# Performance work log

Measured on AMD Instinct MI355X. Metric: run time of the kernel, lower is better.

The kernel has to match this reference:

```python
import jax, jax.numpy as jnp
import numpy as np
from jax import lax

T, H, F, E, K = 4096, 1024, 2048, 8, 2

def setup_inputs() -> dict:
    key = jax.random.key(0)
    k1, k2, k3, k4 = jax.random.split(key, 4)
    return {
        "hidden_states": jax.random.normal(k1, (T, H), jnp.float32),
        "gate_w": jax.random.normal(k2, (E, H), jnp.float32) * 0.02,
        "w1": jax.random.normal(k3, (E, 2 * F, H), jnp.float32) * 0.02,  # fused gate+up
        "w2": jax.random.normal(k4, (E, H, F), jnp.float32) * 0.02,      # down proj
        "top_k": K,
    }

def reference(hidden_states, gate_w, w1, w2, top_k):
    tokens = hidden_states.shape[0]
    # Router gate (Linear, no bias)
    router_logits = hidden_states @ gate_w.T                     # [T, E]
    probs = jax.nn.softmax(router_logits.astype(jnp.float32), axis=-1)
    topk_w, topk_idx = lax.top_k(probs, top_k)                   # [T, K]
    topk_w = topk_w / jnp.sum(topk_w, axis=-1, keepdims=True)    # renormalize
    # Dense combine weights [T, E] (zero for unselected experts)
    combine = jnp.zeros_like(probs).at[jnp.arange(tokens)[:, None], topk_idx].add(topk_w)
    combine = combine.astype(hidden_states.dtype)

    def expert_step(acc, ew):
        w1_e, w2_e, c_e = ew                                     # [2F,H], [H,F], [T]
        h = hidden_states @ w1_e.T                               # [T, 2F]
        g, u = jnp.split(h, 2, axis=-1)
        y = (jax.nn.silu(g) * u) @ w2_e.T                        # [T, H]
        return acc + c_e[:, None] * y, None

    acc0 = jnp.zeros_like(hidden_states)
    final_hidden_states, _ = lax.scan(expert_step, acc0, (w1, w2, combine.T))
    return final_hidden_states, router_logits
```

## Files before the change

kernel.cpp:

```cpp
#include <hip/hip_runtime.h>

#define T 4096
#define Hdim 1024
#define Fdim 2048
#define NE 8
#define TOPK 2
#define TK (T*TOPK)

typedef unsigned short ushort_t;
typedef __attribute__((ext_vector_type(8))) short bf16x8;
typedef __attribute__((ext_vector_type(4))) float floatx4;

__device__ __forceinline__ ushort_t f2bf(float f) {
    unsigned u = __float_as_uint(f);
    u += 0x7fff + ((u >> 16) & 1);
    return (ushort_t)(u >> 16);
}
__device__ __forceinline__ uint4 cvt8(const float4 a, const float4 b) {
    uint4 r;
    r.x = (unsigned)f2bf(a.x) | ((unsigned)f2bf(a.y) << 16);
    r.y = (unsigned)f2bf(a.z) | ((unsigned)f2bf(a.w) << 16);
    r.z = (unsigned)f2bf(b.x) | ((unsigned)f2bf(b.y) << 16);
    r.w = (unsigned)f2bf(b.z) | ((unsigned)f2bf(b.w) << 16);
    return r;
}
__device__ __forceinline__ void gld16(const ushort_t* g, short* l) {
    __builtin_amdgcn_global_load_lds((const __attribute__((address_space(1))) void*)g,
                                     (__attribute__((address_space(3))) void*)l, 16, 0, 0);
}

__global__ __launch_bounds__(256) void cvt_kernel(const float* __restrict__ src,
                                                  ushort_t* __restrict__ dst)
{
    long i = (long)blockIdx.x * 256 + threadIdx.x;
    float4 a = *(const float4*)(src + i * 8);
    float4 b = *(const float4*)(src + i * 8 + 4);
    *(uint4*)(dst + i * 8) = cvt8(a, b);
}

__global__ __launch_bounds__(64) void router_kernel(
    const float* __restrict__ hs, const float* __restrict__ gw,
    float* __restrict__ logits_out, float* __restrict__ out,
    ushort_t* __restrict__ hsb,
    int2* __restrict__ choice, float2* __restrict__ cwt, int* __restrict__ counts)
{
    const int t = blockIdx.x;
    const int lane = threadIdx.x;
    if (t == 0 && lane < NE) counts[lane] = 0;

    float hreg[16];
#pragma unroll
    for (int i = 0; i < 16; ++i)
        hreg[i] = hs[(long)t * Hdim + lane + 64 * i];

#pragma unroll
    for (int i = 0; i < 16; ++i)
        hsb[(long)t * Hdim + lane + 64 * i] = f2bf(hreg[i]);

    const float4 z4 = make_float4(0.f, 0.f, 0.f, 0.f);
#pragma unroll
    for (int i = 0; i < 4; ++i)
        *(float4*)&out[(long)t * Hdim + lane * 4 + 256 * i] = z4;

    float acc[NE];
#pragma unroll
    for (int e = 0; e < NE; ++e) {
        float s = 0.f;
#pragma unroll
        for (int i = 0; i < 16; ++i)
            s += hreg[i] * gw[e * Hdim + lane + 64 * i];
#pragma unroll
        for (int off = 32; off > 0; off >>= 1)
            s += __shfl_xor(s, off, 64);
        acc[e] = s;
    }

    if (lane < NE) logits_out[t * NE + lane] = acc[lane];

    if (lane == 0) {
        int i1 = 0;
#pragma unroll
        for (int e = 1; e < NE; ++e) if (acc[e] > acc[i1]) i1 = e;
        int i2 = -1;
#pragma unroll
        for (int e = 0; e < NE; ++e) {
            if (e == i1) continue;
            if (i2 < 0 || acc[e] > acc[i2]) i2 = e;
        }
        float p2 = __expf(acc[i2] - acc[i1]);
        float z  = 1.f + p2;
        choice[t] = make_int2(i1, i2);
        cwt[t]    = make_float2(1.f / z, p2 / z);
    }
}

__global__ __launch_bounds__(256) void scatter_kernel(
    const int2* __restrict__ choice, const float2* __restrict__ cwt,
    int* __restrict__ counts, int* __restrict__ tok_slot, float* __restrict__ tok_wt)
{
    __shared__ int lhist[NE];
    __shared__ int lbase[NE];
    __shared__ int lpos[NE];
    const int tid = threadIdx.x;
    if (tid < NE) { lhist[tid] = 0; lpos[tid] = 0; }
    __syncthreads();

    const int t = blockIdx.x * 256 + tid;
    int2   ch = choice[t];
    float2 wv = cwt[t];
    atomicAdd(&lhist[ch.x], 1);
    atomicAdd(&lhist[ch.y], 1);
    __syncthreads();

    if (tid < NE) lbase[tid] = atomicAdd(&counts[tid], lhist[tid]);
    __syncthreads();

    int p1 = atomicAdd(&lpos[ch.x], 1);
    int p2 = atomicAdd(&lpos[ch.y], 1);
    int o1 = lbase[ch.x] + p1;
    int o2 = lbase[ch.y] + p2;
    tok_slot[ch.x * T + o1] = t * TOPK + 0;
    tok_wt [ch.x * T + o1] = wv.x;
    tok_slot[ch.y * T + o2] = t * TOPK + 1;
    tok_wt [ch.y * T + o2] = wv.y;
}

__global__ __launch_bounds__(512) void gemm1_kernel(
    const ushort_t* __restrict__ hsb, const ushort_t* __restrict__ w1b,
    const int* __restrict__ counts, const int* __restrict__ tok_slot,
    ushort_t* __restrict__ actb)
{
    const int e = blockIdx.z;
    const int cnt = counts[e];
    const int row0 = blockIdx.y * 256;
    if (row0 >= cnt) return;
    const int f0 = blockIdx.x * 128;

    __shared__ short As[2][256 * 64];
    __shared__ short Bs[2][256 * 64];
    __shared__ int slotLds[256];

    const int tid = threadIdx.x;
    if (tid < 256) {
        int idx = row0 + tid;
        slotLds[tid] = (idx < cnt) ? tok_slot[e * T + idx] : -1;
    }
    __syncthreads();

    const ushort_t* srcA[4];
    const ushort_t* srcB[4];
#pragma unroll
    for (int i = 0; i < 4; ++i) {
        int ci = i * 512 + tid;
        int r  = ci >> 3;
        int gc = (ci & 7) ^ (r & 7);
        int s  = slotLds[r];
        srcA[i] = hsb + (long)(s >= 0 ? (s >> 1) : 0) * Hdim + gc * 8;
        long frow = (r < 128) ? (long)(f0 + r) : (long)(Fdim + f0 + (r - 128));
        srcB[i] = w1b + ((long)e * 2 * Fdim + frow) * Hdim + gc * 8;
    }

    const int lane = tid & 63;
    const int w = tid >> 6;
    const int wm = (w >> 1) * 64;
    const int fn = (w & 1) * 64;
    const int fr = lane & 15, fg = lane >> 4;
    const int cs0 = (fg ^ (fr & 7)) * 8;
    const int cs1 = ((4 + fg) ^ (fr & 7)) * 8;

    floatx4 accg[4][4] = {};
    floatx4 accu[4][4] = {};

#pragma unroll
    for (int i = 0; i < 4; ++i) {
        gld16(srcA[i], &As[0][(i * 512 + tid) * 8]);
        gld16(srcB[i], &Bs[0][(i * 512 + tid) * 8]);
    }
    __syncthreads();

    const int NT = Hdim / 64;
    for (int t = 0; t < NT; ++t) {
        short* Ac = As[t & 1];
        short* Bc = Bs[t & 1];
        short* An = As[(t & 1) ^ 1];
        short* Bn = Bs[(t & 1) ^ 1];
        const bool pf = (t + 1 < NT);
        const long k1 = (long)(t + 1) * 64;

        bf16x8 a[4], b[4];

#pragma unroll
        for (int ms = 0; ms < 4; ++ms)
            a[ms] = *(const bf16x8*)&Ac[(wm + ms * 16 + fr) * 64 + cs0];
#pragma unroll
        for (int ns = 0; ns < 4; ++ns)
            b[ns] = *(const bf16x8*)&Bc[(fn + ns * 16 + fr) * 64 + cs0];
        if (pf) {
            gld16(srcA[0] + k1, &An[(0 * 512 + tid) * 8]);
            gld16(srcB[0] + k1, &Bn[(0 * 512 + tid) * 8]);
        }
        __builtin_amdgcn_s_barrier();
        __builtin_amdgcn_s_setprio(1);
#pragma unroll
        for (int ms = 0; ms < 4; ++ms)
#pragma unroll
            for (int ns = 0; ns < 4; ++ns)
                accg[ms][ns] = __builtin_amdgcn_mfma_f32_16x16x32_bf16(a[ms], b[ns], accg[ms][ns], 0, 0, 0);
        __builtin_amdgcn_s_setprio(0);
        __builtin_amdgcn_s_barrier();

#pragma unroll
        for (int ns = 0; ns < 4; ++ns)
            b[ns] = *(const bf16x8*)&Bc[(128 + fn + ns * 16 + fr) * 64 + cs0];
        if (pf) {
            gld16(srcA[1] + k1, &An[(1 * 512 + tid) * 8]);
            gld16(srcB[1] + k1, &Bn[(1 * 512 + tid) * 8]);
        }
        __builtin_amdgcn_s_barrier();
        __builtin_amdgcn_s_setprio(1);
#pragma unroll
        for (int ms = 0; ms < 4; ++ms)
#pragma unroll
            for (int ns = 0; ns < 4; ++ns)
                accu[ms][ns] = __builtin_amdgcn_mfma_f32_16x16x32_bf16(a[ms], b[ns], accu[ms][ns], 0, 0, 0);
        __builtin_amdgcn_s_setprio(0);
        __builtin_amdgcn_s_barrier();

#pragma unroll
        for (int ms = 0; ms < 4; ++ms)
            a[ms] = *(const bf16x8*)&Ac[(wm + ms * 16 + fr) * 64 + cs1];
#pragma unroll
        for (int ns = 0; ns < 4; ++ns)
            b[ns] = *(const bf16x8*)&Bc[(fn + ns * 16 + fr) * 64 + cs1];
        if (pf) {
            gld16(srcA[2] + k1, &An[(2 * 512 + tid) * 8]);
            gld16(srcB[2] + k1, &Bn[(2 * 512 + tid) * 8]);
        }
        __builtin_amdgcn_s_barrier();
        __builtin_amdgcn_s_setprio(1);
#pragma unroll
        for (int ms = 0; ms < 4; ++ms)
#pragma unroll
            for (int ns = 0; ns < 4; ++ns)
                accg[ms][ns] = __builtin_amdgcn_mfma_f32_16x16x32_bf16(a[ms], b[ns], accg[ms][ns], 0, 0, 0);
        __builtin_amdgcn_s_setprio(0);
        __builtin_amdgcn_s_barrier();

#pragma unroll
        for (int ns = 0; ns < 4; ++ns)
            b[ns] = *(const bf16x8*)&Bc[(128 + fn + ns * 16 + fr) * 64 + cs1];
        if (pf) {
            gld16(srcA[3] + k1, &An[(3 * 512 + tid) * 8]);
            gld16(srcB[3] + k1, &Bn[(3 * 512 + tid) * 8]);
        }
        __builtin_amdgcn_s_barrier();
        __builtin_amdgcn_s_setprio(1);
#pragma unroll
        for (int ms = 0; ms < 4; ++ms)
#pragma unroll
            for (int ns = 0; ns < 4; ++ns)
                accu[ms][ns] = __builtin_amdgcn_mfma_f32_16x16x32_bf16(a[ms], b[ns], accu[ms][ns], 0, 0, 0);
        __builtin_amdgcn_s_setprio(0);
        __builtin_amdgcn_sched_barrier(0);
        asm volatile("s_waitcnt vmcnt(0)" ::: "memory");
        __builtin_amdgcn_s_barrier();
    }

#pragma unroll
    for (int ms = 0; ms < 4; ++ms)
#pragma unroll
        for (int ns = 0; ns < 4; ++ns)
#pragma unroll
            for (int j = 0; j < 4; ++j) {
                int m = wm + ms * 16 + fg * 4 + j;
                int slot = slotLds[m];
                if (slot >= 0) {
                    int fcol = f0 + fn + ns * 16 + fr;
                    float gv = accg[ms][ns][j];
                    float uv = accu[ms][ns][j];
                    float av = (gv / (1.f + __expf(-gv))) * uv;
                    actb[(long)slot * Fdim + fcol] = f2bf(av);
                }
            }
}

__global__ __launch_bounds__(512) void gemm2_kernel(
    const ushort_t* __restrict__ actb, const ushort_t* __restrict__ w2b,
    const int* __restrict__ counts, const int* __restrict__ tok_slot,
    const float* __restrict__ tok_wt, float* __restrict__ out)
{
    const int e = blockIdx.z;
    const int cnt = counts[e];
    const int row0 = blockIdx.y * 128;
    if (row0 >= cnt) return;
    const int h0 = blockIdx.x * 128;

    __shared__ short As[128 * 64];
    __shared__ short Bs[128 * 64];
    __shared__ int   slotLds[128];
    __shared__ float wtLds[128];

    const int tid = threadIdx.x;
    if (tid < 128) {
        int idx = row0 + tid;
        bool ok = idx < cnt;
        slotLds[tid] = ok ? tok_slot[e * T + idx] : -1;
        wtLds[tid]   = ok ? tok_wt [e * T + idx] : 0.f;
    }
    __syncthreads();

    const ushort_t* srcA[2];
    const ushort_t* srcB[2];
#pragma unroll
    for (int i = 0; i < 2; ++i) {
        int ci = i * 512 + tid;
        int r  = ci >> 3;
        int gc = (ci & 7) ^ (r & 7);
        int s  = slotLds[r];
        srcA[i] = actb + (long)(s >= 0 ? s : 0) * Fdim + gc * 8;
        srcB[i] = w2b + ((long)e * Hdim + (h0 + r)) * Fdim + gc * 8;
    }

    const int lane = tid & 63;
    const int w = tid >> 6;
    const int wm = (w >> 2) * 64;
    const int wn = (w & 3) * 32;
    const int fr = lane & 15, fg = lane >> 4;
    const int cs0 = (fg ^ (fr & 7)) * 8;
    const int cs1 = ((4 + fg) ^ (fr & 7)) * 8;

    floatx4 acc[4][2] = {};

    for (int k0 = 0; k0 < Fdim; k0 += 64) {
        __syncthreads();
        gld16(srcA[0] + k0, &As[tid * 8]);
        gld16(srcA[1] + k0, &As[(512 + tid) * 8]);
        gld16(srcB[0] + k0, &Bs[tid * 8]);
        gld16(srcB[1] + k0, &Bs[(512 + tid) * 8]);
        __syncthreads();

#pragma unroll
        for (int kk = 0; kk < 2; ++kk) {
            const int cs = kk ? cs1 : cs0;
            bf16x8 a[4], b[2];
#pragma unroll
            for (int ms = 0; ms < 4; ++ms)
                a[ms] = *(bf16x8*)&As[(wm + ms * 16 + fr) * 64 + cs];
#pragma unroll
            for (int ns = 0; ns < 2; ++ns)
                b[ns] = *(bf16x8*)&Bs[(wn + ns * 16 + fr) * 64 + cs];
#pragma unroll
            for (int ms = 0; ms < 4; ++ms)
#pragma unroll
                for (int ns = 0; ns < 2; ++ns)
                    acc[ms][ns] = __builtin_amdgcn_mfma_f32_16x16x32_bf16(a[ms], b[ns], acc[ms][ns], 0, 0, 0);
        }
    }

#pragma unroll
    for (int ms = 0; ms < 4; ++ms)
#pragma unroll
        for (int ns = 0; ns < 2; ++ns)
#pragma unroll
            for (int j = 0; j < 4; ++j) {
                int m = wm + ms * 16 + fg * 4 + j;
                int slot = slotLds[m];
                if (slot >= 0) {
                    int hcol = h0 + wn + ns * 16 + fr;
                    atomicAdd(&out[(long)(slot >> 1) * Hdim + hcol],
                              acc[ms][ns][j] * wtLds[m]);
                }
            }
}

extern "C" void kernel_launch(void* const* d_in, const int* in_sizes, int n_in,
                              void* d_out, int out_size, void* d_ws, size_t ws_size,
                              hipStream_t stream)
{
    const float* hs = (const float*)d_in[0];
    const float* gw = (const float*)d_in[1];
    const float* w1 = (const float*)d_in[2];
    const float* w2 = (const float*)d_in[3];

    float* out        = (float*)d_out;
    float* logits_out = out + (long)T * Hdim;

    char* ws = (char*)d_ws;
    size_t off = 0;
    int* counts = (int*)(ws + off);          off += 256;
    int* tok_slot = (int*)(ws + off);        off += (size_t)NE * T * sizeof(int);
    float* tok_wt = (float*)(ws + off);      off += (size_t)NE * T * sizeof(float);
    off = (off + 255) & ~(size_t)255;
    ushort_t* hsb = (ushort_t*)(ws + off);   off += (size_t)T * Hdim * sizeof(ushort_t);
    off = (off + 255) & ~(size_t)255;
    char* w1region = ws + off;               off += (size_t)NE * 2 * Fdim * Hdim * sizeof(ushort_t);
    ushort_t* w1b = (ushort_t*)w1region;
    ushort_t* w2b = (ushort_t*)w1region;
    off = (off + 255) & ~(size_t)255;
    ushort_t* actb = (ushort_t*)(ws + off);  off += (size_t)TK * Fdim * sizeof(ushort_t);
    int2*   choice = (int2*)actb;
    float2* cwt    = (float2*)((char*)actb + (size_t)T * sizeof(int2));

    const long n8_w1 = (long)NE * 2 * Fdim * Hdim / 8;
    const long n8_w2 = (long)NE * Hdim * Fdim / 8;

    cvt_kernel<<<(int)(n8_w1 / 256), 256, 0, stream>>>(w1, w1b);
    router_kernel<<<T, 64, 0, stream>>>(hs, gw, logits_out, out, hsb, choice, cwt, counts);
    scatter_kernel<<<T / 256, 256, 0, stream>>>(choice, cwt, counts, tok_slot, tok_wt);
    gemm1_kernel<<<dim3(Fdim / 128, T / 256, NE), 512, 0, stream>>>(hsb, w1b, counts, tok_slot, actb);
    cvt_kernel<<<(int)(n8_w2 / 256), 256, 0, stream>>>(w2, w2b);
    gemm2_kernel<<<dim3(Hdim / 128, T / 128, NE), 512, 0, stream>>>(actb, w2b, counts, tok_slot, tok_wt, out);
}
```

Baseline: 433.9 us.

## Restructure gemm1 pipeline with single barrier pair; double-buffer and enlarge gemm2 tiles

In gemm1, all next-tile prefetch loads are now issued at the start of each K-step, followed by a partial vmcnt wait and a barrier. This replaces the four barrier pairs interleaved with the MFMA groups, so each iteration does its LDS reads and MFMAs without intermediate barriers. gemm2 moves from a single-buffered 128x128 tile with two syncthreads per step to a double-buffered 256x128 tile with asynchronous prefetch, 64x64 per-wave subtiles and larger accumulators. The aim is to overlap global loads with compute and raise MFMA reuse. The cost is more LDS and registers per block, which may lower occupancy, and the partial waits depend on how vmcnt counts the LDS-direct loads.

```diff
diff --git a/kernel.cpp b/kernel.cpp
--- a/kernel.cpp
+++ b/kernel.cpp
@@ -176,7 +176,6 @@
         gld16(srcA[i], &As[0][(i * 512 + tid) * 8]);
         gld16(srcB[i], &Bs[0][(i * 512 + tid) * 8]);
     }
-    __syncthreads();
 
     const int NT = Hdim / 64;
     for (int t = 0; t < NT; ++t) {
@@ -187,83 +186,50 @@
         const bool pf = (t + 1 < NT);
         const long k1 = (long)(t + 1) * 64;
 
+        __builtin_amdgcn_sched_barrier(0);
+        __builtin_amdgcn_s_barrier();
+        if (pf) {
+#pragma unroll
+            for (int i = 0; i < 4; ++i) {
+                gld16(srcA[i] + k1, &An[(i * 512 + tid) * 8]);
+                gld16(srcB[i] + k1, &Bn[(i * 512 + tid) * 8]);
+            }
+            asm volatile("s_waitcnt vmcnt(8)" ::: "memory");
+        } else {
+            asm volatile("s_waitcnt vmcnt(0)" ::: "memory");
+        }
+        __builtin_amdgcn_sched_barrier(0);
+        __builtin_amdgcn_s_barrier();
+        __builtin_amdgcn_sched_barrier(0);
+
         bf16x8 a[4], b[4];
-
-#pragma unroll
-        for (int ms = 0; ms < 4; ++ms)
-            a[ms] = *(const bf16x8*)&Ac[(wm + ms * 16 + fr) * 64 + cs0];
-#pragma unroll
-        for (int ns = 0; ns < 4; ++ns)
-            b[ns] = *(const bf16x8*)&Bc[(fn + ns * 16 + fr) * 64 + cs0];
-        if (pf) {
-            gld16(srcA[0] + k1, &An[(0 * 512 + tid) * 8]);
-            gld16(srcB[0] + k1, &Bn[(0 * 512 + tid) * 8]);
+#pragma unroll
+        for (int kk = 0; kk < 2; ++kk) {
+            const int cs = kk ? cs1 : cs0;
+#pragma unroll
+            for (int ms = 0; ms < 4; ++ms)
+                a[ms] = *(const bf16x8*)&Ac[(wm + ms * 16 + fr) * 64 + cs];
+#pragma unroll
+            for (int ns = 0; ns < 4; ++ns)
+                b[ns] = *(const bf16x8*)&Bc[(fn + ns * 16 + fr) * 64 + cs];
+            __builtin_amdgcn_s_setprio(1);
+#pragma unroll
+            for (int ms = 0; ms < 4; ++ms)
+#pragma unroll
+                for (int ns = 0; ns < 4; ++ns)
+                    accg[ms][ns] = __builtin_amdgcn_mfma_f32_16x16x32_bf16(a[ms], b[ns], accg[ms][ns], 0, 0, 0);
+            __builtin_amdgcn_s_setprio(0);
+#pragma unroll
+            for (int ns = 0; ns < 4; ++ns)
+                b[ns] = *(const bf16x8*)&Bc[(128 + fn + ns * 16 + fr) * 64 + cs];
+            __builtin_amdgcn_s_setprio(1);
+#pragma unroll
+            for (int ms = 0; ms < 4; ++ms)
+#pragma unroll
+                for (int ns = 0; ns < 4; ++ns)
+                    accu[ms][ns] = __builtin_amdgcn_mfma_f32_16x16x32_bf16(a[ms], b[ns], accu[ms][ns], 0, 0, 0);
+            __builtin_amdgcn_s_setprio(0);
         }
-        __builtin_amdgcn_s_barrier();
-        __builtin_amdgcn_s_setprio(1);
-#pragma unroll
-        for (int ms = 0; ms < 4; ++ms)
-#pragma unroll
-            for (int ns = 0; ns < 4; ++ns)
-                accg[ms][ns] = __builtin_amdgcn_mfma_f32_16x16x32_bf16(a[ms], b[ns], accg[ms][ns], 0, 0, 0);
-        __builtin_amdgcn_s_setprio(0);
-        __builtin_amdgcn_s_barrier();
-
-#pragma unroll
-        for (int ns = 0; ns < 4; ++ns)
-            b[ns] = *(const bf16x8*)&Bc[(128 + fn + ns * 16 + fr) * 64 + cs0];
-        if (pf) {
-            gld16(srcA[1] + k1, &An[(1 * 512 + tid) * 8]);
-            gld16(srcB[1] + k1, &Bn[(1 * 512 + tid) * 8]);
-        }
-        __builtin_amdgcn_s_barrier();
-        __builtin_amdgcn_s_setprio(1);
-#pragma unroll
-        for (int ms = 0; ms < 4; ++ms)
-#pragma unroll
-            for (int ns = 0; ns < 4; ++ns)
-                accu[ms][ns] = __builtin_amdgcn_mfma_f32_16x16x32_bf16(a[ms], b[ns], accu[ms][ns], 0, 0, 0);
-        __builtin_amdgcn_s_setprio(0);
-        __builtin_amdgcn_s_barrier();
-
-#pragma unroll
-        for (int ms = 0; ms < 4; ++ms)
-            a[ms] = *(const bf16x8*)&Ac[(wm + ms * 16 + fr) * 64 + cs1];
-#pragma unroll
-        for (int ns = 0; ns < 4; ++ns)
-            b[ns] = *(const bf16x8*)&Bc[(fn + ns * 16 + fr) * 64 + cs1];
-        if (pf) {
-            gld16(srcA[2] + k1, &An[(2 * 512 + tid) * 8]);
-            gld16(srcB[2] + k1, &Bn[(2 * 512 + tid) * 8]);
-        }
-        __builtin_amdgcn_s_barrier();
-        __builtin_amdgcn_s_setprio(1);
-#pragma unroll
-        for (int ms = 0; ms < 4; ++ms)
-#pragma unroll
-            for (int ns = 0; ns < 4; ++ns)
-                accg[ms][ns] = __builtin_amdgcn_mfma_f32_16x16x32_bf16(a[ms], b[ns], accg[ms][ns], 0, 0, 0);
-        __builtin_amdgcn_s_setprio(0);
-        __builtin_amdgcn_s_barrier();
-
-#pragma unroll
-        for (int ns = 0; ns < 4; ++ns)
-            b[ns] = *(const bf16x8*)&Bc[(128 + fn + ns * 16 + fr) * 64 + cs1];
-        if (pf) {
-            gld16(srcA[3] + k1, &An[(3 * 512 + tid) * 8]);
-            gld16(srcB[3] + k1, &Bn[(3 * 512 + tid) * 8]);
-        }
-        __builtin_amdgcn_s_barrier();
-        __builtin_amdgcn_s_setprio(1);
-#pragma unroll
-        for (int ms = 0; ms < 4; ++ms)
-#pragma unroll
-            for (int ns = 0; ns < 4; ++ns)
-                accu[ms][ns] = __builtin_amdgcn_mfma_f32_16x16x32_bf16(a[ms], b[ns], accu[ms][ns], 0, 0, 0);
-        __builtin_amdgcn_s_setprio(0);
-        __builtin_amdgcn_sched_barrier(0);
-        asm volatile("s_waitcnt vmcnt(0)" ::: "memory");
-        __builtin_amdgcn_s_barrier();
     }
 
 #pragma unroll
@@ -291,17 +257,17 @@
 {
     const int e = blockIdx.z;
     const int cnt = counts[e];
-    const int row0 = blockIdx.y * 128;
+    const int row0 = blockIdx.y * 256;
     if (row0 >= cnt) return;
     const int h0 = blockIdx.x * 128;
 
-    __shared__ short As[128 * 64];
-    __shared__ short Bs[128 * 64];
-    __shared__ int   slotLds[128];
-    __shared__ float wtLds[128];
+    __shared__ short As[2][256 * 64];
+    __shared__ short Bs[2][128 * 64];
+    __shared__ int   slotLds[256];
+    __shared__ float wtLds[256];
 
     const int tid = threadIdx.x;
-    if (tid < 128) {
+    if (tid < 256) {
         int idx = row0 + tid;
         bool ok = idx < cnt;
         slotLds[tid] = ok ? tok_slot[e * T + idx] : -1;
@@ -309,58 +275,87 @@
     }
     __syncthreads();
 
-    const ushort_t* srcA[2];
+    const ushort_t* srcA[4];
     const ushort_t* srcB[2];
 #pragma unroll
-    for (int i = 0; i < 2; ++i) {
+    for (int i = 0; i < 4; ++i) {
         int ci = i * 512 + tid;
         int r  = ci >> 3;
         int gc = (ci & 7) ^ (r & 7);
         int s  = slotLds[r];
         srcA[i] = actb + (long)(s >= 0 ? s : 0) * Fdim + gc * 8;
+    }
+#pragma unroll
+    for (int i = 0; i < 2; ++i) {
+        int ci = i * 512 + tid;
+        int r  = ci >> 3;
+        int gc = (ci & 7) ^ (r & 7);
         srcB[i] = w2b + ((long)e * Hdim + (h0 + r)) * Fdim + gc * 8;
     }
 
     const int lane = tid & 63;
     const int w = tid >> 6;
-    const int wm = (w >> 2) * 64;
-    const int wn = (w & 3) * 32;
+    const int wm = (w >> 1) * 64;
+    const int wn = (w & 1) * 64;
     const int fr = lane & 15, fg = lane >> 4;
     const int cs0 = (fg ^ (fr & 7)) * 8;
     const int cs1 = ((4 + fg) ^ (fr & 7)) * 8;
 
-    floatx4 acc[4][2] = {};
-
-    for (int k0 = 0; k0 < Fdim; k0 += 64) {
-        __syncthreads();
-        gld16(srcA[0] + k0, &As[tid * 8]);
-        gld16(srcA[1] + k0, &As[(512 + tid) * 8]);
-        gld16(srcB[0] + k0, &Bs[tid * 8]);
-        gld16(srcB[1] + k0, &Bs[(512 + tid) * 8]);
-        __syncthreads();
-
+    floatx4 acc[4][4] = {};
+
+#pragma unroll
+    for (int i = 0; i < 4; ++i) gld16(srcA[i], &As[0][(i * 512 + tid) * 8]);
+#pragma unroll
+    for (int i = 0; i < 2; ++i) gld16(srcB[i], &Bs[0][(i * 512 + tid) * 8]);
+
+    const int NT = Fdim / 64;
+    for (int t = 0; t < NT; ++t) {
+        short* Ac = As[t & 1];
+        short* Bc = Bs[t & 1];
+        short* An = As[(t & 1) ^ 1];
+        short* Bn = Bs[(t & 1) ^ 1];
+        const bool pf = (t + 1 < NT);
+        const long k1 = (long)(t + 1) * 64;
+
+        __builtin_amdgcn_sched_barrier(0);
+        __builtin_amdgcn_s_barrier();
+        if (pf) {
+#pragma unroll
+            for (int i = 0; i < 4; ++i) gld16(srcA[i] + k1, &An[(i * 512 + tid) * 8]);
+#pragma unroll
+            for (int i = 0; i < 2; ++i) gld16(srcB[i] + k1, &Bn[(i * 512 + tid) * 8]);
+            asm volatile("s_waitcnt vmcnt(6)" ::: "memory");
+        } else {
+            asm volatile("s_waitcnt vmcnt(0)" ::: "memory");
+        }
+        __builtin_amdgcn_sched_barrier(0);
+        __builtin_amdgcn_s_barrier();
+        __builtin_amdgcn_sched_barrier(0);
+
+        bf16x8 a[4], b[4];
 #pragma unroll
         for (int kk = 0; kk < 2; ++kk) {
             const int cs = kk ? cs1 : cs0;
-            bf16x8 a[4], b[2];
 #pragma unroll
             for (int ms = 0; ms < 4; ++ms)
-                a[ms] = *(bf16x8*)&As[(wm + ms * 16 + fr) * 64 + cs];
-#pragma unroll
-            for (int ns = 0; ns < 2; ++ns)
-                b[ns] = *(bf16x8*)&Bs[(wn + ns * 16 + fr) * 64 + cs];
+                a[ms] = *(const bf16x8*)&Ac[(wm + ms * 16 + fr) * 64 + cs];
+#pragma unroll
+            for (int ns = 0; ns < 4; ++ns)
+                b[ns] = *(const bf16x8*)&Bc[(wn + ns * 16 + fr) * 64 + cs];
+            __builtin_amdgcn_s_setprio(1);
 #pragma unroll
             for (int ms = 0; ms < 4; ++ms)
 #pragma unroll
-                for (int ns = 0; ns < 2; ++ns)
+                for (int ns = 0; ns < 4; ++ns)
                     acc[ms][ns] = __builtin_amdgcn_mfma_f32_16x16x32_bf16(a[ms], b[ns], acc[ms][ns], 0, 0, 0);
+            __builtin_amdgcn_s_setprio(0);
         }
     }
 
 #pragma unroll
     for (int ms = 0; ms < 4; ++ms)
 #pragma unroll
-        for (int ns = 0; ns < 2; ++ns)
+        for (int ns = 0; ns < 4; ++ns)
 #pragma unroll
             for (int j = 0; j < 4; ++j) {
                 int m = wm + ms * 16 + fg * 4 + j;
@@ -409,5 +404,5 @@
     scatter_kernel<<<T / 256, 256, 0, stream>>>(choice, cwt, counts, tok_slot, tok_wt);
     gemm1_kernel<<<dim3(Fdim / 128, T / 256, NE), 512, 0, stream>>>(hsb, w1b, counts, tok_slot, actb);
     cvt_kernel<<<(int)(n8_w2 / 256), 256, 0, stream>>>(w2, w2b);
-    gemm2_kernel<<<dim3(Hdim / 128, T / 128, NE), 512, 0, stream>>>(actb, w2b, counts, tok_slot, tok_wt, out);
-}
+    gemm2_kernel<<<dim3(Hdim / 128, T / 256, NE), 512, 0, stream>>>(actb, w2b, counts, tok_slot, tok_wt, out);
+}
```

After: 479.2 us. +10.4%, slower.

## Software-pipeline LDS fragment loads across MFMA phases in gate/up GEMM

Applied to the files above, without the earlier changes.

Restructures the gate/up GEMM main loop to double-buffer register fragments (a0/a1, bg/bu). Each phase's LDS reads are issued before the previous phase's MFMAs, with partial lgkmcnt waits, so LDS latency overlaps compute. Global prefetches are grouped into two batches, and the next tile's first fragments are loaded after a single full barrier per iteration. This costs more VGPRs and leans on manual waitcnt values that must match the actual instruction ordering.

```diff
diff --git a/kernel.cpp b/kernel.cpp
--- a/kernel.cpp
+++ b/kernel.cpp
@@ -170,100 +170,111 @@
 
     floatx4 accg[4][4] = {};
     floatx4 accu[4][4] = {};
+    bf16x8 a0[4], a1[4], bg[4], bu[4];
 
 #pragma unroll
     for (int i = 0; i < 4; ++i) {
         gld16(srcA[i], &As[0][(i * 512 + tid) * 8]);
         gld16(srcB[i], &Bs[0][(i * 512 + tid) * 8]);
     }
-    __syncthreads();
+    asm volatile("s_waitcnt vmcnt(0)" ::: "memory");
+    __builtin_amdgcn_s_barrier();
+    __builtin_amdgcn_sched_barrier(0);
+#pragma unroll
+    for (int ms = 0; ms < 4; ++ms)
+        a0[ms] = *(const bf16x8*)&As[0][(wm + ms * 16 + fr) * 64 + cs0];
+#pragma unroll
+    for (int ns = 0; ns < 4; ++ns)
+        bg[ns] = *(const bf16x8*)&Bs[0][(fn + ns * 16 + fr) * 64 + cs0];
+    __builtin_amdgcn_sched_barrier(0);
 
     const int NT = Hdim / 64;
     for (int t = 0; t < NT; ++t) {
-        short* Ac = As[t & 1];
-        short* Bc = Bs[t & 1];
+        const short* Ac = As[t & 1];
+        const short* Bc = Bs[t & 1];
         short* An = As[(t & 1) ^ 1];
         short* Bn = Bs[(t & 1) ^ 1];
         const bool pf = (t + 1 < NT);
         const long k1 = (long)(t + 1) * 64;
 
-        bf16x8 a[4], b[4];
-
+        if (pf) {
+#pragma unroll
+            for (int i = 0; i < 4; ++i)
+                gld16(srcA[i] + k1, &An[(i * 512 + tid) * 8]);
+        }
+#pragma unroll
+        for (int ns = 0; ns < 4; ++ns)
+            bu[ns] = *(const bf16x8*)&Bc[(128 + fn + ns * 16 + fr) * 64 + cs0];
+        __builtin_amdgcn_sched_barrier(0);
+        __builtin_amdgcn_s_barrier();
+        asm volatile("s_waitcnt lgkmcnt(4)" ::: "memory");
+        __builtin_amdgcn_sched_barrier(0);
+        __builtin_amdgcn_s_setprio(1);
 #pragma unroll
         for (int ms = 0; ms < 4; ++ms)
-            a[ms] = *(const bf16x8*)&Ac[(wm + ms * 16 + fr) * 64 + cs0];
+#pragma unroll
+            for (int ns = 0; ns < 4; ++ns)
+                accg[ms][ns] = __builtin_amdgcn_mfma_f32_16x16x32_bf16(a0[ms], bg[ns], accg[ms][ns], 0, 0, 0);
+        __builtin_amdgcn_s_setprio(0);
+
+        if (pf) {
+#pragma unroll
+            for (int i = 0; i < 4; ++i)
+                gld16(srcB[i] + k1, &Bn[(i * 512 + tid) * 8]);
+        }
+#pragma unroll
+        for (int ms = 0; ms < 4; ++ms)
+            a1[ms] = *(const bf16x8*)&Ac[(wm + ms * 16 + fr) * 64 + cs1];
 #pragma unroll
         for (int ns = 0; ns < 4; ++ns)
-            b[ns] = *(const bf16x8*)&Bc[(fn + ns * 16 + fr) * 64 + cs0];
+            bg[ns] = *(const bf16x8*)&Bc[(fn + ns * 16 + fr) * 64 + cs1];
+        __builtin_amdgcn_sched_barrier(0);
+        __builtin_amdgcn_s_barrier();
+        asm volatile("s_waitcnt lgkmcnt(8)" ::: "memory");
+        __builtin_amdgcn_sched_barrier(0);
+        __builtin_amdgcn_s_setprio(1);
+#pragma unroll
+        for (int ms = 0; ms < 4; ++ms)
+#pragma unroll
+            for (int ns = 0; ns < 4; ++ns)
+                accu[ms][ns] = __builtin_amdgcn_mfma_f32_16x16x32_bf16(a0[ms], bu[ns], accu[ms][ns], 0, 0, 0);
+        __builtin_amdgcn_s_setprio(0);
+
+#pragma unroll
+        for (int ns = 0; ns < 4; ++ns)
+            bu[ns] = *(const bf16x8*)&Bc[(128 + fn + ns * 16 + fr) * 64 + cs1];
+        __builtin_amdgcn_sched_barrier(0);
+        __builtin_amdgcn_s_barrier();
+        asm volatile("s_waitcnt lgkmcnt(4)" ::: "memory");
+        __builtin_amdgcn_sched_barrier(0);
+        __builtin_amdgcn_s_setprio(1);
+#pragma unroll
+        for (int ms = 0; ms < 4; ++ms)
+#pragma unroll
+            for (int ns = 0; ns < 4; ++ns)
+                accg[ms][ns] = __builtin_amdgcn_mfma_f32_16x16x32_bf16(a1[ms], bg[ns], accg[ms][ns], 0, 0, 0);
+        __builtin_amdgcn_s_setprio(0);
+
+        __builtin_amdgcn_sched_barrier(0);
+        asm volatile("s_waitcnt vmcnt(0) lgkmcnt(0)" ::: "memory");
+        __builtin_amdgcn_s_barrier();
+        __builtin_amdgcn_sched_barrier(0);
         if (pf) {
-            gld16(srcA[0] + k1, &An[(0 * 512 + tid) * 8]);
-            gld16(srcB[0] + k1, &Bn[(0 * 512 + tid) * 8]);
+#pragma unroll
+            for (int ms = 0; ms < 4; ++ms)
+                a0[ms] = *(const bf16x8*)&An[(wm + ms * 16 + fr) * 64 + cs0];
+#pragma unroll
+            for (int ns = 0; ns < 4; ++ns)
+                bg[ns] = *(const bf16x8*)&Bn[(fn + ns * 16 + fr) * 64 + cs0];
         }
-        __builtin_amdgcn_s_barrier();
+        __builtin_amdgcn_sched_barrier(0);
         __builtin_amdgcn_s_setprio(1);
 #pragma unroll
         for (int ms = 0; ms < 4; ++ms)
 #pragma unroll
             for (int ns = 0; ns < 4; ++ns)
-                accg[ms][ns] = __builtin_amdgcn_mfma_f32_16x16x32_bf16(a[ms], b[ns], accg[ms][ns], 0, 0, 0);
+                accu[ms][ns] = __builtin_amdgcn_mfma_f32_16x16x32_bf16(a1[ms], bu[ns], accu[ms][ns], 0, 0, 0);
         __builtin_amdgcn_s_setprio(0);
-        __builtin_amdgcn_s_barrier();
-
-#pragma unroll
-        for (int ns = 0; ns < 4; ++ns)
-            b[ns] = *(const bf16x8*)&Bc[(128 + fn + ns * 16 + fr) * 64 + cs0];
-        if (pf) {
-            gld16(srcA[1] + k1, &An[(1 * 512 + tid) * 8]);
-            gld16(srcB[1] + k1, &Bn[(1 * 512 + tid) * 8]);
-        }
-        __builtin_amdgcn_s_barrier();
-        __builtin_amdgcn_s_setprio(1);
-#pragma unroll
-        for (int ms = 0; ms < 4; ++ms)
-#pragma unroll
-            for (int ns = 0; ns < 4; ++ns)
-                accu[ms][ns] = __builtin_amdgcn_mfma_f32_16x16x32_bf16(a[ms], b[ns], accu[ms][ns], 0, 0, 0);
-        __builtin_amdgcn_s_setprio(0);
-        __builtin_amdgcn_s_barrier();
-
-#pragma unroll
-        for (int ms = 0; ms < 4; ++ms)
-            a[ms] = *(const bf16x8*)&Ac[(wm + ms * 16 + fr) * 64 + cs1];
-#pragma unroll
-        for (int ns = 0; ns < 4; ++ns)
-            b[ns] = *(const bf16x8*)&Bc[(fn + ns * 16 + fr) * 64 + cs1];
-        if (pf) {
-            gld16(srcA[2] + k1, &An[(2 * 512 + tid) * 8]);
-            gld16(srcB[2] + k1, &Bn[(2 * 512 + tid) * 8]);
-        }
-        __builtin_amdgcn_s_barrier();
-        __builtin_amdgcn_s_setprio(1);
-#pragma unroll
-        for (int ms = 0; ms < 4; ++ms)
-#pragma unroll
-            for (int ns = 0; ns < 4; ++ns)
-                accg[ms][ns] = __builtin_amdgcn_mfma_f32_16x16x32_bf16(a[ms], b[ns], accg[ms][ns], 0, 0, 0);
-        __builtin_amdgcn_s_setprio(0);
-        __builtin_amdgcn_s_barrier();
-
-#pragma unroll
-        for (int ns = 0; ns < 4; ++ns)
-            b[ns] = *(const bf16x8*)&Bc[(128 + fn + ns * 16 + fr) * 64 + cs1];
-        if (pf) {
-            gld16(srcA[3] + k1, &An[(3 * 512 + tid) * 8]);
-            gld16(srcB[3] + k1, &Bn[(3 * 512 + tid) * 8]);
-        }
-        __builtin_amdgcn_s_barrier();
-        __builtin_amdgcn_s_setprio(1);
-#pragma unroll
-        for (int ms = 0; ms < 4; ++ms)
-#pragma unroll
-            for (int ns = 0; ns < 4; ++ns)
-                accu[ms][ns] = __builtin_amdgcn_mfma_f32_16x16x32_bf16(a[ms], b[ns], accu[ms][ns], 0, 0, 0);
-        __builtin_amdgcn_s_setprio(0);
-        __builtin_amdgcn_sched_barrier(0);
-        asm volatile("s_waitcnt vmcnt(0)" ::: "memory");
-        __builtin_amdgcn_s_barrier();
     }
 
 #pragma unroll
```

Result: no change. 437.6 us (+0.9%).

## Fuse w1 bf16 conversion into gemm1 loads and w2 conversion into gemm1 prologue

Applied to the files above, without the earlier changes.

Drops both standalone fp32-to-bf16 weight conversion kernels. gemm1 now reads w1 as fp32, converts it in registers and stores the bf16 values to LDS through a register-staged prefetch. Every gemm1 block also converts a slice of w2 to bf16 for gemm2 before any early exit, so the full w2 is covered. This removes a full-size write and re-read of bf16 w1 and two launches. In exchange gemm1 loads twice the bytes for B, spends VALU time converting, and each w1 tile is re-converted by every token-row block of the same expert.

```diff
diff --git a/kernel.cpp b/kernel.cpp
--- a/kernel.cpp
+++ b/kernel.cpp
@@ -27,15 +27,6 @@
 __device__ __forceinline__ void gld16(const ushort_t* g, short* l) {
     __builtin_amdgcn_global_load_lds((const __attribute__((address_space(1))) void*)g,
                                      (__attribute__((address_space(3))) void*)l, 16, 0, 0);
-}
-
-__global__ __launch_bounds__(256) void cvt_kernel(const float* __restrict__ src,
-                                                  ushort_t* __restrict__ dst)
-{
-    long i = (long)blockIdx.x * 256 + threadIdx.x;
-    float4 a = *(const float4*)(src + i * 8);
-    float4 b = *(const float4*)(src + i * 8 + 4);
-    *(uint4*)(dst + i * 8) = cvt8(a, b);
 }
 
 __global__ __launch_bounds__(64) void router_kernel(
@@ -126,10 +117,24 @@
 }
 
 __global__ __launch_bounds__(512) void gemm1_kernel(
-    const ushort_t* __restrict__ hsb, const ushort_t* __restrict__ w1b,
+    const ushort_t* __restrict__ hsb, const float* __restrict__ w1,
+    const float* __restrict__ w2, ushort_t* __restrict__ w2b,
     const int* __restrict__ counts, const int* __restrict__ tok_slot,
     ushort_t* __restrict__ actb)
 {
+    const int tid = threadIdx.x;
+
+    {
+        int lin = ((int)blockIdx.z * 16 + (int)blockIdx.y) * 16 + (int)blockIdx.x;
+        long base = (long)lin * 8192 + (long)tid * 16;
+        float4 x0 = *(const float4*)(w2 + base);
+        float4 x1 = *(const float4*)(w2 + base + 4);
+        float4 x2 = *(const float4*)(w2 + base + 8);
+        float4 x3 = *(const float4*)(w2 + base + 12);
+        *(uint4*)(w2b + base)     = cvt8(x0, x1);
+        *(uint4*)(w2b + base + 8) = cvt8(x2, x3);
+    }
+
     const int e = blockIdx.z;
     const int cnt = counts[e];
     const int row0 = blockIdx.y * 256;
@@ -140,7 +145,6 @@
     __shared__ short Bs[2][256 * 64];
     __shared__ int slotLds[256];
 
-    const int tid = threadIdx.x;
     if (tid < 256) {
         int idx = row0 + tid;
         slotLds[tid] = (idx < cnt) ? tok_slot[e * T + idx] : -1;
@@ -148,7 +152,8 @@
     __syncthreads();
 
     const ushort_t* srcA[4];
-    const ushort_t* srcB[4];
+    const float* srcBf[4];
+    int bDst[4];
 #pragma unroll
     for (int i = 0; i < 4; ++i) {
         int ci = i * 512 + tid;
@@ -157,7 +162,8 @@
         int s  = slotLds[r];
         srcA[i] = hsb + (long)(s >= 0 ? (s >> 1) : 0) * Hdim + gc * 8;
         long frow = (r < 128) ? (long)(f0 + r) : (long)(Fdim + f0 + (r - 128));
-        srcB[i] = w1b + ((long)e * 2 * Fdim + frow) * Hdim + gc * 8;
+        srcBf[i] = w1 + ((long)e * 2 * Fdim + frow) * Hdim + gc * 8;
+        bDst[i]  = ci * 8;
     }
 
     const int lane = tid & 63;
@@ -172,16 +178,26 @@
     floatx4 accu[4][4] = {};
 
 #pragma unroll
-    for (int i = 0; i < 4; ++i) {
+    for (int i = 0; i < 4; ++i)
         gld16(srcA[i], &As[0][(i * 512 + tid) * 8]);
-        gld16(srcB[i], &Bs[0][(i * 512 + tid) * 8]);
-    }
-    __syncthreads();
-
+    {
+        float4 p[8];
+#pragma unroll
+        for (int i = 0; i < 4; ++i) {
+            p[2 * i]     = *(const float4*)(srcBf[i]);
+            p[2 * i + 1] = *(const float4*)(srcBf[i] + 4);
+        }
+#pragma unroll
+        for (int i = 0; i < 4; ++i)
+            *(uint4*)&Bs[0][bDst[i]] = cvt8(p[2 * i], p[2 * i + 1]);
+    }
+    __syncthreads();
+
+    float4 br[8];
     const int NT = Hdim / 64;
     for (int t = 0; t < NT; ++t) {
-        short* Ac = As[t & 1];
-        short* Bc = Bs[t & 1];
+        const short* Ac = As[t & 1];
+        const short* Bc = Bs[t & 1];
         short* An = As[(t & 1) ^ 1];
         short* Bn = Bs[(t & 1) ^ 1];
         const bool pf = (t + 1 < NT);
@@ -196,8 +212,14 @@
         for (int ns = 0; ns < 4; ++ns)
             b[ns] = *(const bf16x8*)&Bc[(fn + ns * 16 + fr) * 64 + cs0];
         if (pf) {
-            gld16(srcA[0] + k1, &An[(0 * 512 + tid) * 8]);
-            gld16(srcB[0] + k1, &Bn[(0 * 512 + tid) * 8]);
+#pragma unroll
+            for (int i = 0; i < 4; ++i)
+                gld16(srcA[i] + k1, &An[(i * 512 + tid) * 8]);
+#pragma unroll
+            for (int i = 0; i < 4; ++i) {
+                br[2 * i]     = *(const float4*)(srcBf[i] + k1);
+                br[2 * i + 1] = *(const float4*)(srcBf[i] + k1 + 4);
+            }
         }
         __builtin_amdgcn_s_barrier();
         __builtin_amdgcn_s_setprio(1);
@@ -212,10 +234,6 @@
 #pragma unroll
         for (int ns = 0; ns < 4; ++ns)
             b[ns] = *(const bf16x8*)&Bc[(128 + fn + ns * 16 + fr) * 64 + cs0];
-        if (pf) {
-            gld16(srcA[1] + k1, &An[(1 * 512 + tid) * 8]);
-            gld16(srcB[1] + k1, &Bn[(1 * 512 + tid) * 8]);
-        }
         __builtin_amdgcn_s_barrier();
         __builtin_amdgcn_s_setprio(1);
 #pragma unroll
@@ -226,16 +244,17 @@
         __builtin_amdgcn_s_setprio(0);
         __builtin_amdgcn_s_barrier();
 
+        if (pf) {
+#pragma unroll
+            for (int i = 0; i < 4; ++i)
+                *(uint4*)&Bn[bDst[i]] = cvt8(br[2 * i], br[2 * i + 1]);
+        }
 #pragma unroll
         for (int ms = 0; ms < 4; ++ms)
             a[ms] = *(const bf16x8*)&Ac[(wm + ms * 16 + fr) * 64 + cs1];
 #pragma unroll
         for (int ns = 0; ns < 4; ++ns)
             b[ns] = *(const bf16x8*)&Bc[(fn + ns * 16 + fr) * 64 + cs1];
-        if (pf) {
-            gld16(srcA[2] + k1, &An[(2 * 512 + tid) * 8]);
-            gld16(srcB[2] + k1, &Bn[(2 * 512 + tid) * 8]);
-        }
         __builtin_amdgcn_s_barrier();
         __builtin_amdgcn_s_setprio(1);
 #pragma unroll
@@ -249,10 +268,6 @@
 #pragma unroll
         for (int ns = 0; ns < 4; ++ns)
             b[ns] = *(const bf16x8*)&Bc[(128 + fn + ns * 16 + fr) * 64 + cs1];
-        if (pf) {
-            gld16(srcA[3] + k1, &An[(3 * 512 + tid) * 8]);
-            gld16(srcB[3] + k1, &Bn[(3 * 512 + tid) * 8]);
-        }
         __builtin_amdgcn_s_barrier();
         __builtin_amdgcn_s_setprio(1);
 #pragma unroll
@@ -262,7 +277,7 @@
                 accu[ms][ns] = __builtin_amdgcn_mfma_f32_16x16x32_bf16(a[ms], b[ns], accu[ms][ns], 0, 0, 0);
         __builtin_amdgcn_s_setprio(0);
         __builtin_amdgcn_sched_barrier(0);
-        asm volatile("s_waitcnt vmcnt(0)" ::: "memory");
+        asm volatile("s_waitcnt vmcnt(0) lgkmcnt(0)" ::: "memory");
         __builtin_amdgcn_s_barrier();
     }
 
@@ -393,21 +408,14 @@
     off = (off + 255) & ~(size_t)255;
     ushort_t* hsb = (ushort_t*)(ws + off);   off += (size_t)T * Hdim * sizeof(ushort_t);
     off = (off + 255) & ~(size_t)255;
-    char* w1region = ws + off;               off += (size_t)NE * 2 * Fdim * Hdim * sizeof(ushort_t);
-    ushort_t* w1b = (ushort_t*)w1region;
-    ushort_t* w2b = (ushort_t*)w1region;
+    ushort_t* w2b = (ushort_t*)(ws + off);   off += (size_t)NE * Hdim * Fdim * sizeof(ushort_t);
     off = (off + 255) & ~(size_t)255;
     ushort_t* actb = (ushort_t*)(ws + off);  off += (size_t)TK * Fdim * sizeof(ushort_t);
     int2*   choice = (int2*)actb;
     float2* cwt    = (float2*)((char*)actb + (size_t)T * sizeof(int2));
 
-    const long n8_w1 = (long)NE * 2 * Fdim * Hdim / 8;
-    const long n8_w2 = (long)NE * Hdim * Fdim / 8;
-
-    cvt_kernel<<<(int)(n8_w1 / 256), 256, 0, stream>>>(w1, w1b);
     router_kernel<<<T, 64, 0, stream>>>(hs, gw, logits_out, out, hsb, choice, cwt, counts);
     scatter_kernel<<<T / 256, 256, 0, stream>>>(choice, cwt, counts, tok_slot, tok_wt);
-    gemm1_kernel<<<dim3(Fdim / 128, T / 256, NE), 512, 0, stream>>>(hsb, w1b, counts, tok_slot, actb);
-    cvt_kernel<<<(int)(n8_w2 / 256), 256, 0, stream>>>(w2, w2b);
+    gemm1_kernel<<<dim3(Fdim / 128, T / 256, NE), 512, 0, stream>>>(hsb, w1, w2, w2b, counts, tok_slot, actb);
     gemm2_kernel<<<dim3(Hdim / 128, T / 128, NE), 512, 0, stream>>>(actb, w2b, counts, tok_slot, tok_wt, out);
 }
```

New measurement: 463.5 us. +6.8%, slower.
